# Performance work log

Measured on AMD Instinct MI355X. Metric: run time of the kernel, lower is better.

## Reference

```python
import jax, jax.numpy as jnp
import numpy as np

K = 16          # top-k edges kept per node (init kwarg k)
TEMP = 1.0      # gumbel-softmax temperature
NEG = -1e9


def setup_inputs() -> dict:
    key = jax.random.key(0)
    ks = jax.random.split(key, 12)
    N, E, D, ED, H1, H2, OUT = 4096, 131072, 8, 8, 16, 16, 112
    x = jax.random.normal(ks[0], (N, D), jnp.float32)
    edge_index = jax.random.randint(ks[1], (2, E), 0, N, dtype=jnp.int64)
    edge_attr = jax.random.normal(ks[2], (E, ED), jnp.float32)
    node_mask = jnp.ones((N,), jnp.int32)
    # learned params
    mlp_w = jax.random.normal(ks[3], (1, ED + 2 * D), jnp.float32) * 0.1
    mlp_b = jnp.zeros((1,), jnp.float32)
    w1 = jax.random.normal(ks[4], (D, H1), jnp.float32) * (1.0 / np.sqrt(D))
    b1 = jnp.zeros((H1,), jnp.float32)
    w2 = jax.random.normal(ks[5], (H1, H2), jnp.float32) * (1.0 / np.sqrt(H1))
    b2 = jnp.zeros((H2,), jnp.float32)
    fc_w = jax.random.normal(ks[6], (H2, OUT), jnp.float32) * (1.0 / np.sqrt(H2))
    fc_b = jnp.zeros((OUT,), jnp.float32)
    return {"num_nodes": N, "edge_index": edge_index, "edge_attr": edge_attr,
            "x": x, "node_mask": node_mask, "mlp_w": mlp_w, "mlp_b": mlp_b,
            "w1": w1, "b1": b1, "w2": w2, "b2": b2, "fc_w": fc_w, "fc_b": fc_b}


def reference(num_nodes, edge_index, edge_attr, x, node_mask,
              mlp_w, mlp_b, w1, b1, w2, b2, fc_w, fc_b):
    N = num_nodes
    D = x.shape[1]
    row, col = edge_index[0], edge_index[1]

    # dense adjacency indicator (original: sparse_coo -> to_dense; used only via adj != 0)
    adj = jnp.zeros((N, N), x.dtype).at[row, col].set(1.0)

    # Linear MLP over concat([node_emb, neighbor_emb, edge_emb]) decomposes:
    # score[u,v] = x_u.w_node + adj[u,v]*(x_v.w_nbr) + (e_uv.w_edge) + b
    w_node = mlp_w[0, :D]
    w_nbr = mlp_w[0, D:2 * D]
    w_edge = mlp_w[0, 2 * D:]
    edge_s = jnp.zeros((N, N), x.dtype).at[row, col].set(edge_attr @ w_edge)
    score = (x @ w_node)[:, None] + adj * (x @ w_nbr)[None, :] + edge_s + mlp_b[0]

    score = jnp.where(adj > 0, score, NEG)
    z = jax.nn.softmax(score, axis=-1)
    z = jnp.where(adj > 0, z, NEG)
    # eval mode: gumbel noise = 0
    z = jax.nn.softmax(z / TEMP, axis=-1)

    vals, idx = jax.lax.top_k(z, K)          # (N, K)
    kth = vals[:, -1]
    topk_mask = jnp.zeros((N, N), bool).at[jnp.arange(N)[:, None], idx].set(True)

    # per-edge keep mask -> expressed as edge weight 0/1 (static shapes)
    keep = (node_mask[row] != 0) & (kth[row] != 0) & topk_mask[row, col]
    w_e = keep.astype(x.dtype)

    def gcn_conv(h, W, b):
        hW = h @ W
        deg = jnp.zeros((N,), h.dtype).at[col].add(w_e) + 1.0   # +1 self loop
        dinv = jax.lax.rsqrt(deg)
        coef = w_e * dinv[row] * dinv[col]
        agg = jnp.zeros((N, hW.shape[1]), h.dtype).at[col].add(coef[:, None] * hW[row])
        return agg + (dinv * dinv)[:, None] * hW + b            # self-loop term + bias

    # GCN (eval mode => dropout is identity)
    h = jax.nn.relu(gcn_conv(x, w1, b1))
    h = gcn_conv(h, w2, b2)
    h = jax.nn.relu(h)
    out = h @ fc_w + fc_b
    # node_mask is all ones, so x[node_mask != 0] == x
    return out
```

## Files before the change

kernel.cpp:

```cpp
#include <hip/hip_runtime.h>
#include <stdint.h>

#define N_NODES 4096
#define N_EDGES 131072
#define D_IN    8
#define NH      16
#define N_OUT   112
#define TOPK    16
#define CAP_ROW 128
#define CAP_COL 64

__global__ __launch_bounds__(256) void k_pre(
        const int* __restrict__ ei, const float* __restrict__ ea,
        const float* __restrict__ x, const float* __restrict__ mlp_w,
        const float* __restrict__ w1,
        float* __restrict__ s_nbr, float* __restrict__ h1W,
        int* __restrict__ deg_row, unsigned* __restrict__ csr,
        float* __restrict__ csr_ew) {
    int b = blockIdx.x;
    if (b < N_EDGES / 256) {
        int e = b * 256 + threadIdx.x;
        const float4* ea4 = (const float4*)ea;
        float4 a0 = ea4[2 * e], a1 = ea4[2 * e + 1];
        float s = a0.x * mlp_w[16] + a0.y * mlp_w[17] + a0.z * mlp_w[18] +
                  a0.w * mlp_w[19] + a1.x * mlp_w[20] + a1.y * mlp_w[21] +
                  a1.z * mlp_w[22] + a1.w * mlp_w[23];
        int r = ei[e];
        int c = ei[N_EDGES + e];
        int slot = atomicAdd(&deg_row[r], 1);
        if (slot < CAP_ROW) {
            csr[r * CAP_ROW + slot] = ((unsigned)e << 12) | (unsigned)c;
            csr_ew[r * CAP_ROW + slot] = s;
        }
    } else {
        int i = (b - N_EDGES / 256) * 256 + threadIdx.x;
        if (i >= N_NODES) return;
        const float4* x4 = (const float4*)x;
        float4 v0 = x4[2 * i], v1 = x4[2 * i + 1];
        float xv[D_IN] = {v0.x, v0.y, v0.z, v0.w, v1.x, v1.y, v1.z, v1.w};
        float s = 0.f;
#pragma unroll
        for (int d = 0; d < D_IN; ++d) s += xv[d] * mlp_w[D_IN + d];
        s_nbr[i] = s;
#pragma unroll
        for (int j = 0; j < NH; ++j) {
            float a = 0.f;
#pragma unroll
            for (int d = 0; d < D_IN; ++d) a += xv[d] * w1[d * NH + j];
            h1W[i * NH + j] = a;
        }
    }
}

__global__ __launch_bounds__(64) void k_topk(
        const unsigned* __restrict__ csr, const float* __restrict__ csr_ew,
        const int* __restrict__ deg_row, const float* __restrict__ s_nbr,
        const int* __restrict__ node_mask,
        int* __restrict__ deg_in, int* __restrict__ csc) {
    __shared__ unsigned s_pk[CAP_ROW];
    __shared__ float s_v[CAP_ROW];
    __shared__ unsigned char s_rep[CAP_ROW];
    __shared__ unsigned char s_kept[CAP_ROW];
    __shared__ int s_distinct;
    int r = blockIdx.x;
    int t = threadIdx.x;
    int n = deg_row[r];
    if (n > CAP_ROW) n = CAP_ROW;
    if (n == 0) return;
    for (int k = t; k < n; k += 64) {
        unsigned pk = csr[r * CAP_ROW + k];
        s_pk[k] = pk;
        s_v[k] = s_nbr[pk & 4095u] + csr_ew[r * CAP_ROW + k];
    }
    __syncthreads();
    for (int k = t; k < n; k += 64) {
        unsigned pk = s_pk[k], c = pk & 4095u;
        unsigned char rep = 1;
        for (int j = 0; j < n; ++j) {
            unsigned pj = s_pk[j];
            if ((pj & 4095u) == c && pj > pk) { rep = 0; break; }
        }
        s_rep[k] = rep;
    }
    __syncthreads();
    if (t == 0) {
        int c = 0;
        for (int j = 0; j < n; ++j) c += s_rep[j];
        s_distinct = c;
    }
    __syncthreads();
    if (s_distinct < TOPK || node_mask[r] == 0) return;
    for (int k = t; k < n; k += 64) {
        unsigned char kept = 0;
        if (s_rep[k]) {
            float vk = s_v[k];
            unsigned ck = s_pk[k] & 4095u;
            int beats = 0;
            for (int j = 0; j < n; ++j) {
                if (!s_rep[j]) continue;
                float vj = s_v[j];
                unsigned cj = s_pk[j] & 4095u;
                if (vj > vk || (vj == vk && cj < ck)) ++beats;
            }
            kept = (beats < TOPK);
        }
        s_kept[k] = kept;
    }
    __syncthreads();
    for (int k = t; k < n; k += 64) {
        unsigned c = s_pk[k] & 4095u;
        unsigned char kp = 0;
        for (int j = 0; j < n; ++j) {
            if ((s_pk[j] & 4095u) == c && s_rep[j]) { kp = s_kept[j]; break; }
        }
        if (kp) {
            int p = atomicAdd(&deg_in[(int)c], 1);
            if (p < CAP_COL) csc[(int)c * CAP_COL + p] = r;
        }
    }
}

__global__ __launch_bounds__(256) void k_gather1(
        const int* __restrict__ csc, const int* __restrict__ deg_in,
        const float* __restrict__ h1W, const float* __restrict__ b1,
        const float* __restrict__ w2, float* __restrict__ h2W) {
    const int lane = threadIdx.x & 63;
    const int c = blockIdx.x * 4 + (threadIdx.x >> 6);
    const int f = lane & 15;
    const int jj = lane >> 4;
    const int m = deg_in[c];
    const int mm = m > CAP_COL ? CAP_COL : m;
    float acc = 0.f;
    for (int j = jj; j < mm; j += 4) {
        int r = csc[c * CAP_COL + j];
        acc += rsqrtf(1.0f + (float)deg_in[r]) * h1W[r * NH + f];
    }
    acc += __shfl_xor(acc, 16, 64);
    acc += __shfl_xor(acc, 32, 64);
    const float dc = rsqrtf(1.0f + (float)m);
    float v = dc * acc + dc * dc * h1W[c * NH + f] + b1[f];
    float h = v > 0.f ? v : 0.f;
    float a = 0.f;
#pragma unroll
    for (int ff = 0; ff < NH; ++ff) {
        float hv = __shfl(h, ff, 64);
        a += hv * w2[ff * NH + f];
    }
    if (jj == 0) h2W[c * NH + f] = a;
}

__global__ __launch_bounds__(256) void k_out(
        const int* __restrict__ csc, const int* __restrict__ deg_in,
        const float* __restrict__ h2W, const float* __restrict__ b2,
        const float* __restrict__ fc_w, const float* __restrict__ fc_b,
        float* __restrict__ out) {
    const int lane = threadIdx.x & 63;
    const int c = blockIdx.x * 4 + (threadIdx.x >> 6);
    const int f = lane & 15;
    const int jj = lane >> 4;
    const int m = deg_in[c];
    const int mm = m > CAP_COL ? CAP_COL : m;
    float acc = 0.f;
    for (int j = jj; j < mm; j += 4) {
        int r = csc[c * CAP_COL + j];
        acc += rsqrtf(1.0f + (float)deg_in[r]) * h2W[r * NH + f];
    }
    acc += __shfl_xor(acc, 16, 64);
    acc += __shfl_xor(acc, 32, 64);
    const float dc = rsqrtf(1.0f + (float)m);
    float v = dc * acc + dc * dc * h2W[c * NH + f] + b2[f];
    float h = v > 0.f ? v : 0.f;
    float a0 = fc_b[lane];
    float a1 = (lane < N_OUT - 64) ? fc_b[64 + lane] : 0.f;
#pragma unroll
    for (int ff = 0; ff < NH; ++ff) {
        float hv = __shfl(h, ff, 64);
        a0 += hv * fc_w[ff * N_OUT + lane];
        if (lane < N_OUT - 64) a1 += hv * fc_w[ff * N_OUT + 64 + lane];
    }
    out[c * N_OUT + lane] = a0;
    if (lane < N_OUT - 64) out[c * N_OUT + 64 + lane] = a1;
}

extern "C" void kernel_launch(void* const* d_in, const int* in_sizes, int n_in,
                              void* d_out, int out_size, void* d_ws, size_t ws_size,
                              hipStream_t stream) {
    const int*   ei        = (const int*)d_in[1];
    const float* ea        = (const float*)d_in[2];
    const float* x         = (const float*)d_in[3];
    const int*   node_mask = (const int*)d_in[4];
    const float* mlp_w     = (const float*)d_in[5];
    const float* w1        = (const float*)d_in[7];
    const float* b1        = (const float*)d_in[8];
    const float* w2        = (const float*)d_in[9];
    const float* b2        = (const float*)d_in[10];
    const float* fcw       = (const float*)d_in[11];
    const float* fcb       = (const float*)d_in[12];
    float* out = (float*)d_out;

    char* ws = (char*)d_ws;
    size_t off = 0;
    auto alloc = [&](size_t bytes) -> void* {
        void* p = ws + off;
        off += (bytes + 511) & ~(size_t)511;
        return p;
    };
    int*      deg_row = (int*)alloc(N_NODES * 4);
    int*      deg_in  = (int*)alloc(N_NODES * 4);
    size_t zero_bytes = off;
    float*    s_nbr  = (float*)alloc(N_NODES * 4);
    float*    h1W    = (float*)alloc(N_NODES * NH * 4);
    float*    h2W    = (float*)alloc(N_NODES * NH * 4);
    unsigned* csr    = (unsigned*)alloc(N_NODES * CAP_ROW * 4);
    float*    csr_ew = (float*)alloc(N_NODES * CAP_ROW * 4);
    int*      csc    = (int*)alloc(N_NODES * CAP_COL * 4);
    (void)ws_size; (void)in_sizes; (void)n_in; (void)out_size;

    hipMemsetAsync(d_ws, 0, zero_bytes, stream);

    k_pre<<<N_EDGES / 256 + N_NODES / 256, 256, 0, stream>>>(
        ei, ea, x, mlp_w, w1, s_nbr, h1W, deg_row, csr, csr_ew);
    k_topk<<<N_NODES, 64, 0, stream>>>(
        csr, csr_ew, deg_row, s_nbr, node_mask, deg_in, csc);
    k_gather1<<<N_NODES / 4, 256, 0, stream>>>(
        csc, deg_in, h1W, b1, w2, h2W);
    k_out<<<N_NODES / 4, 256, 0, stream>>>(
        csc, deg_in, h2W, b2, fcw, fcb, out);
}
```

Baseline: 133.8 us.

## Pack CSR entries, use wave-reduce count, prescale h2W, unroll gathers

Packs each row-CSR entry's column and edge score into one uint2 so k_pre does a single store and k_topk a single load. k_topk counts distinct neighbors with a wave shuffle reduction instead of a serial thread-0 loop plus a barrier, and representative entries read their own keep flag directly. k_gather1 prescales h2W by the destination degree factor so k_out's gather drops the per-neighbor deg_in lookup and rsqrt. Both gather loops are unrolled by two to expose more memory-level parallelism. These are several independent micro-optimizations, and the prescaling reorders floating-point operations slightly.

```diff
diff --git a/kernel.cpp b/kernel.cpp
--- a/kernel.cpp
+++ b/kernel.cpp
@@ -15,8 +15,7 @@
         const float* __restrict__ x, const float* __restrict__ mlp_w,
         const float* __restrict__ w1,
         float* __restrict__ s_nbr, float* __restrict__ h1W,
-        int* __restrict__ deg_row, unsigned* __restrict__ csr,
-        float* __restrict__ csr_ew) {
+        int* __restrict__ deg_row, uint2* __restrict__ csr2) {
     int b = blockIdx.x;
     if (b < N_EDGES / 256) {
         int e = b * 256 + threadIdx.x;
@@ -29,8 +28,10 @@
         int c = ei[N_EDGES + e];
         int slot = atomicAdd(&deg_row[r], 1);
         if (slot < CAP_ROW) {
-            csr[r * CAP_ROW + slot] = ((unsigned)e << 12) | (unsigned)c;
-            csr_ew[r * CAP_ROW + slot] = s;
+            uint2 pk;
+            pk.x = ((unsigned)e << 12) | (unsigned)c;
+            pk.y = __float_as_uint(s);
+            csr2[r * CAP_ROW + slot] = pk;
         }
     } else {
         int i = (b - N_EDGES / 256) * 256 + threadIdx.x;
@@ -53,7 +54,7 @@
 }
 
 __global__ __launch_bounds__(64) void k_topk(
-        const unsigned* __restrict__ csr, const float* __restrict__ csr_ew,
+        const uint2* __restrict__ csr2,
         const int* __restrict__ deg_row, const float* __restrict__ s_nbr,
         const int* __restrict__ node_mask,
         int* __restrict__ deg_in, int* __restrict__ csc) {
@@ -61,16 +62,15 @@
     __shared__ float s_v[CAP_ROW];
     __shared__ unsigned char s_rep[CAP_ROW];
     __shared__ unsigned char s_kept[CAP_ROW];
-    __shared__ int s_distinct;
     int r = blockIdx.x;
     int t = threadIdx.x;
     int n = deg_row[r];
     if (n > CAP_ROW) n = CAP_ROW;
     if (n == 0) return;
     for (int k = t; k < n; k += 64) {
-        unsigned pk = csr[r * CAP_ROW + k];
-        s_pk[k] = pk;
-        s_v[k] = s_nbr[pk & 4095u] + csr_ew[r * CAP_ROW + k];
+        uint2 pv = csr2[r * CAP_ROW + k];
+        s_pk[k] = pv.x;
+        s_v[k] = s_nbr[pv.x & 4095u] + __uint_as_float(pv.y);
     }
     __syncthreads();
     for (int k = t; k < n; k += 64) {
@@ -83,13 +83,11 @@
         s_rep[k] = rep;
     }
     __syncthreads();
-    if (t == 0) {
-        int c = 0;
-        for (int j = 0; j < n; ++j) c += s_rep[j];
-        s_distinct = c;
-    }
-    __syncthreads();
-    if (s_distinct < TOPK || node_mask[r] == 0) return;
+    int cnt = 0;
+    for (int k = t; k < n; k += 64) cnt += s_rep[k];
+#pragma unroll
+    for (int off = 32; off; off >>= 1) cnt += __shfl_xor(cnt, off, 64);
+    if (cnt < TOPK || node_mask[r] == 0) return;
     for (int k = t; k < n; k += 64) {
         unsigned char kept = 0;
         if (s_rep[k]) {
@@ -109,9 +107,14 @@
     __syncthreads();
     for (int k = t; k < n; k += 64) {
         unsigned c = s_pk[k] & 4095u;
-        unsigned char kp = 0;
-        for (int j = 0; j < n; ++j) {
-            if ((s_pk[j] & 4095u) == c && s_rep[j]) { kp = s_kept[j]; break; }
+        unsigned char kp;
+        if (s_rep[k]) {
+            kp = s_kept[k];
+        } else {
+            kp = 0;
+            for (int j = 0; j < n; ++j) {
+                if ((s_pk[j] & 4095u) == c && s_rep[j]) { kp = s_kept[j]; break; }
+            }
         }
         if (kp) {
             int p = atomicAdd(&deg_in[(int)c], 1);
@@ -123,17 +126,29 @@
 __global__ __launch_bounds__(256) void k_gather1(
         const int* __restrict__ csc, const int* __restrict__ deg_in,
         const float* __restrict__ h1W, const float* __restrict__ b1,
-        const float* __restrict__ w2, float* __restrict__ h2W) {
+        const float* __restrict__ w2, float* __restrict__ h2Ws) {
     const int lane = threadIdx.x & 63;
     const int c = blockIdx.x * 4 + (threadIdx.x >> 6);
     const int f = lane & 15;
     const int jj = lane >> 4;
     const int m = deg_in[c];
     const int mm = m > CAP_COL ? CAP_COL : m;
+    const int base = c * CAP_COL;
     float acc = 0.f;
-    for (int j = jj; j < mm; j += 4) {
-        int r = csc[c * CAP_COL + j];
-        acc += rsqrtf(1.0f + (float)deg_in[r]) * h1W[r * NH + f];
+    int j = jj;
+    for (; j + 4 < mm; j += 8) {
+        int r0 = csc[base + j];
+        int r1 = csc[base + j + 4];
+        float d0 = (float)deg_in[r0];
+        float d1 = (float)deg_in[r1];
+        float h0 = h1W[r0 * NH + f];
+        float h1 = h1W[r1 * NH + f];
+        acc += rsqrtf(1.0f + d0) * h0;
+        acc += rsqrtf(1.0f + d1) * h1;
+    }
+    if (j < mm) {
+        int r0 = csc[base + j];
+        acc += rsqrtf(1.0f + (float)deg_in[r0]) * h1W[r0 * NH + f];
     }
     acc += __shfl_xor(acc, 16, 64);
     acc += __shfl_xor(acc, 32, 64);
@@ -146,12 +161,12 @@
         float hv = __shfl(h, ff, 64);
         a += hv * w2[ff * NH + f];
     }
-    if (jj == 0) h2W[c * NH + f] = a;
+    if (jj == 0) h2Ws[c * NH + f] = dc * a;
 }
 
 __global__ __launch_bounds__(256) void k_out(
         const int* __restrict__ csc, const int* __restrict__ deg_in,
-        const float* __restrict__ h2W, const float* __restrict__ b2,
+        const float* __restrict__ h2Ws, const float* __restrict__ b2,
         const float* __restrict__ fc_w, const float* __restrict__ fc_b,
         float* __restrict__ out) {
     const int lane = threadIdx.x & 63;
@@ -160,15 +175,20 @@
     const int jj = lane >> 4;
     const int m = deg_in[c];
     const int mm = m > CAP_COL ? CAP_COL : m;
+    const int base = c * CAP_COL;
     float acc = 0.f;
-    for (int j = jj; j < mm; j += 4) {
-        int r = csc[c * CAP_COL + j];
-        acc += rsqrtf(1.0f + (float)deg_in[r]) * h2W[r * NH + f];
-    }
+    int j = jj;
+    for (; j + 4 < mm; j += 8) {
+        int r0 = csc[base + j];
+        int r1 = csc[base + j + 4];
+        acc += h2Ws[r0 * NH + f];
+        acc += h2Ws[r1 * NH + f];
+    }
+    if (j < mm) acc += h2Ws[csc[base + j] * NH + f];
     acc += __shfl_xor(acc, 16, 64);
     acc += __shfl_xor(acc, 32, 64);
     const float dc = rsqrtf(1.0f + (float)m);
-    float v = dc * acc + dc * dc * h2W[c * NH + f] + b2[f];
+    float v = dc * (acc + h2Ws[c * NH + f]) + b2[f];
     float h = v > 0.f ? v : 0.f;
     float a0 = fc_b[lane];
     float a1 = (lane < N_OUT - 64) ? fc_b[64 + lane] : 0.f;
@@ -210,20 +230,19 @@
     size_t zero_bytes = off;
     float*    s_nbr  = (float*)alloc(N_NODES * 4);
     float*    h1W    = (float*)alloc(N_NODES * NH * 4);
-    float*    h2W    = (float*)alloc(N_NODES * NH * 4);
-    unsigned* csr    = (unsigned*)alloc(N_NODES * CAP_ROW * 4);
-    float*    csr_ew = (float*)alloc(N_NODES * CAP_ROW * 4);
+    float*    h2Ws   = (float*)alloc(N_NODES * NH * 4);
+    uint2*    csr2   = (uint2*)alloc(N_NODES * CAP_ROW * 8);
     int*      csc    = (int*)alloc(N_NODES * CAP_COL * 4);
     (void)ws_size; (void)in_sizes; (void)n_in; (void)out_size;
 
     hipMemsetAsync(d_ws, 0, zero_bytes, stream);
 
     k_pre<<<N_EDGES / 256 + N_NODES / 256, 256, 0, stream>>>(
-        ei, ea, x, mlp_w, w1, s_nbr, h1W, deg_row, csr, csr_ew);
+        ei, ea, x, mlp_w, w1, s_nbr, h1W, deg_row, csr2);
     k_topk<<<N_NODES, 64, 0, stream>>>(
-        csr, csr_ew, deg_row, s_nbr, node_mask, deg_in, csc);
+        csr2, deg_row, s_nbr, node_mask, deg_in, csc);
     k_gather1<<<N_NODES / 4, 256, 0, stream>>>(
-        csc, deg_in, h1W, b1, w2, h2W);
+        csc, deg_in, h1W, b1, w2, h2Ws);
     k_out<<<N_NODES / 4, 256, 0, stream>>>(
-        csc, deg_in, h2W, b2, fcw, fcb, out);
-}
+        csc, deg_in, h2Ws, b2, fcw, fcb, out);
+}
```

After: 123.0 us. -8.1%, faster.
